# Performance work log

Measured on AMD Instinct MI355X. Metric: run time of the kernel, lower is better.

The kernel has to match this reference:

```python
import jax, jax.numpy as jnp
import numpy as np

B, NS, D, H = 1024, 32, 1024, 4096
LN_EPS = 1e-5


def _layer_norm(x, g, b):
    mu = jnp.mean(x, axis=-1, keepdims=True)
    var = jnp.mean(jnp.square(x - mu), axis=-1, keepdims=True)
    return (x - mu) * jax.lax.rsqrt(var + LN_EPS) * g + b


def setup_inputs() -> dict:
    key = jax.random.key(0)
    ks = jax.random.split(key, 12)
    sc = 0.02
    inp = {
        "x": jax.random.normal(ks[0], (B, D), jnp.float32),
        "S": jax.random.normal(ks[1], (B, NS, D), jnp.float32),
        # route_mlp: Linear(2D, D) -> GELU -> Linear(D, NS)
        "w_r1": jax.random.normal(ks[2], (2 * D, D), jnp.float32) * sc,
        "b_r1": jnp.zeros((D,), jnp.float32),
        "w_r2": jax.random.normal(ks[3], (D, NS), jnp.float32) * sc,
        "b_r2": jnp.zeros((NS,), jnp.float32),
        # GRUCell(D, D): gates ordered [r, z, n] as in torch
        "w_ih": jax.random.normal(ks[4], (D, 3 * D), jnp.float32) * sc,
        "w_hh": jax.random.normal(ks[5], (D, 3 * D), jnp.float32) * sc,
        "b_ih": jnp.zeros((3 * D,), jnp.float32),
        "b_hh": jnp.zeros((3 * D,), jnp.float32),
        # slot_proj: Linear(D, D)
        "w_proj": jax.random.normal(ks[6], (D, D), jnp.float32) * sc,
        "b_proj": jnp.zeros((D,), jnp.float32),
        # ln1 / ffn / ln2
        "ln1_g": jnp.ones((D,), jnp.float32),
        "ln1_b": jnp.zeros((D,), jnp.float32),
        "w_f1": jax.random.normal(ks[7], (D, H), jnp.float32) * sc,
        "b_f1": jnp.zeros((H,), jnp.float32),
        "w_f2": jax.random.normal(ks[8], (H, D), jnp.float32) * sc,
        "b_f2": jnp.zeros((D,), jnp.float32),
        "ln2_g": jnp.ones((D,), jnp.float32),
        "ln2_b": jnp.zeros((D,), jnp.float32),
    }
    return inp


def reference(x, S, w_r1, b_r1, w_r2, b_r2, w_ih, w_hh, b_ih, b_hh,
              w_proj, b_proj, ln1_g, ln1_b, w_f1, b_f1, w_f2, b_f2,
              ln2_g, ln2_b):
    tau = 1.0
    # --- context-aware routing ---
    slot_mean = jnp.mean(S, axis=1)                     # [B, D]
    ctx = jnp.concatenate([x, slot_mean], axis=-1)      # [B, 2D]
    h_r = jax.nn.gelu(ctx @ w_r1 + b_r1, approximate=False)
    r_logits = h_r @ w_r2 + b_r2                        # [B, NS]
    alpha = jax.nn.softmax(r_logits / tau, axis=-1)     # [B, NS]

    # --- GRU slot update: input U = alpha * x broadcast over slots ---
    U = alpha[:, :, None] * x[:, None, :]               # [B, NS, D]
    gi = U @ w_ih + b_ih                                # [B, NS, 3D]
    gh = S @ w_hh + b_hh                                # [B, NS, 3D]
    gi_r, gi_z, gi_n = jnp.split(gi, 3, axis=-1)
    gh_r, gh_z, gh_n = jnp.split(gh, 3, axis=-1)
    r = jax.nn.sigmoid(gi_r + gh_r)
    z = jax.nn.sigmoid(gi_z + gh_z)
    n = jnp.tanh(gi_n + r * gh_n)
    S_new = (1.0 - z) * n + z * S                       # [B, NS, D]

    # --- weighted readout (slot_dropout = 0.0) ---
    slot_context = jnp.sum(alpha[:, :, None] * S_new, axis=1)  # [B, D]
    slot_update = slot_context @ w_proj + b_proj
    x_mid = x + slot_update

    # --- FFN + residual + LayerNorms ---
    h = _layer_norm(x_mid, ln1_g, ln1_b)
    ff = jax.nn.gelu(h @ w_f1 + b_f1, approximate=False) @ w_f2 + b_f2
    x_out = _layer_norm(x_mid + ff, ln2_g, ln2_b)
    return (x_out, S_new, alpha)
```

## Files before the change

kernel.cpp:

```cpp
#include <hip/hip_runtime.h>
#include <hip/hip_bf16.h>

#define BB 1024
#define NSLOT 32
#define DD 1024
#define HH 4096

typedef __bf16 bfx8 __attribute__((ext_vector_type(8)));
typedef float f32x4 __attribute__((ext_vector_type(4)));

__device__ __forceinline__ unsigned short f2bfu(float f) {
  union { float f; unsigned u; } v; v.f = f;
  unsigned r = v.u + 0x7fffu + ((v.u >> 16) & 1u);
  return (unsigned short)(r >> 16);
}
__device__ __forceinline__ float bfu2f(unsigned short u) {
  union { unsigned u; float f; } v; v.u = ((unsigned)u) << 16; return v.f;
}
__device__ __forceinline__ float gelu_f(float x) {
  return 0.5f * x * (1.0f + erff(x * 0.70710678118654752f));
}
__device__ __forceinline__ float sigm(float x) { return 1.0f / (1.0f + expf(-x)); }

__device__ __forceinline__ void async16(const unsigned short* g, unsigned short* l) {
  __builtin_amdgcn_global_load_lds(
      (const __attribute__((address_space(1))) unsigned int*)g,
      (__attribute__((address_space(3))) unsigned int*)l, 16, 0, 0);
}


__global__ __launch_bounds__(256) void cvt_x_ctx(const float* __restrict__ x,
                                                 unsigned short* __restrict__ ctx) {
  int i = blockIdx.x * 256 + threadIdx.x;
  int b = i >> 8;
  int c4 = (i & 255) * 4;
  float4 v = ((const float4*)(x + (size_t)b * DD))[i & 255];
  ushort4 o; o.x = f2bfu(v.x); o.y = f2bfu(v.y); o.z = f2bfu(v.z); o.w = f2bfu(v.w);
  *(ushort4*)&ctx[(size_t)b * (2 * DD) + c4] = o;
}

__global__ __launch_bounds__(256) void cvt4(const float* __restrict__ in,
                                            unsigned short* __restrict__ out, int n4) {
  int i = blockIdx.x * 256 + threadIdx.x;
  if (i >= n4) return;
  float4 v = ((const float4*)in)[i];
  ushort4 o; o.x = f2bfu(v.x); o.y = f2bfu(v.y); o.z = f2bfu(v.z); o.w = f2bfu(v.w);
  ((ushort4*)out)[i] = o;
}

__global__ __launch_bounds__(256) void slot_mean_k(const unsigned short* __restrict__ Sb,
                                                   unsigned short* __restrict__ ctx) {
  int i = blockIdx.x * 256 + threadIdx.x;
  int b = i >> 10, d = i & 1023;
  const unsigned short* p = Sb + (size_t)b * NSLOT * DD + d;
  float s = 0.f;
  #pragma unroll
  for (int sl = 0; sl < NSLOT; sl++) s += bfu2f(p[sl * DD]);
  ctx[(size_t)b * (2 * DD) + DD + d] = f2bfu(s * (1.0f / NSLOT));
}

__global__ __launch_bounds__(256) void transp(const float* __restrict__ in,
                                              unsigned short* __restrict__ out,
                                              int R, int C) {
  __shared__ float t[32][33];
  int tx = threadIdx.x & 31, ty = threadIdx.x >> 5;
  int c0 = blockIdx.x * 32, r0 = blockIdx.y * 32;
  #pragma unroll
  for (int i = 0; i < 4; i++) {
    int r = r0 + ty * 4 + i;
    t[ty * 4 + i][tx] = in[(size_t)r * C + c0 + tx];
  }
  __syncthreads();
  #pragma unroll
  for (int i = 0; i < 4; i++) {
    int c = c0 + ty * 4 + i;
    out[(size_t)c * R + r0 + tx] = f2bfu(t[tx][ty * 4 + i]);
  }
}

template <int EPI>
__global__ __launch_bounds__(256) void gemm_nt(
    const unsigned short* __restrict__ A, int lda,
    const unsigned short* __restrict__ Bt, int ldb, int K,
    const float* __restrict__ bias,
    const float* __restrict__ add, int ldadd,
    float* __restrict__ outF, unsigned short* __restrict__ outB, int ldout) {
  __shared__ __align__(16) unsigned short lA[128 * 40];
  __shared__ __align__(16) unsigned short lB[64 * 40];
  const int tid = threadIdx.x;
  const int wave = tid >> 6, lane = tid & 63;
  const int q = lane >> 4, l15 = lane & 15;
  const int row0 = blockIdx.y * 128;
  const int col0 = blockIdx.x * 64;
  const int ar = tid >> 2;
  const int ac = (tid & 3) * 8;

  f32x4 acc[2][4];
  #pragma unroll
  for (int m = 0; m < 2; m++)
    #pragma unroll
    for (int n = 0; n < 4; n++) acc[m][n] = (f32x4){0.f, 0.f, 0.f, 0.f};

  for (int k0 = 0; k0 < K; k0 += 32) {
    *(uint4*)&lA[ar * 40 + ac] = *(const uint4*)&A[(size_t)(row0 + ar) * lda + k0 + ac];
    *(uint4*)&lA[(ar + 64) * 40 + ac] = *(const uint4*)&A[(size_t)(row0 + ar + 64) * lda + k0 + ac];
    *(uint4*)&lB[ar * 40 + ac] = *(const uint4*)&Bt[(size_t)(col0 + ar) * ldb + k0 + ac];
    __syncthreads();
    bfx8 af[2], bf[4];
    #pragma unroll
    for (int m = 0; m < 2; m++)
      af[m] = *(const bfx8*)&lA[(wave * 32 + m * 16 + l15) * 40 + q * 8];
    #pragma unroll
    for (int n = 0; n < 4; n++)
      bf[n] = *(const bfx8*)&lB[(n * 16 + l15) * 40 + q * 8];
    #pragma unroll
    for (int m = 0; m < 2; m++)
      #pragma unroll
      for (int n = 0; n < 4; n++)
        acc[m][n] = __builtin_amdgcn_mfma_f32_16x16x32_bf16(af[m], bf[n], acc[m][n], 0, 0, 0);
    __syncthreads();
  }

  #pragma unroll
  for (int m = 0; m < 2; m++) {
    #pragma unroll
    for (int n = 0; n < 4; n++) {
      int gr0 = row0 + wave * 32 + m * 16 + q * 4;
      int gc = col0 + n * 16 + l15;
      #pragma unroll
      for (int i = 0; i < 4; i++) {
        int gr = gr0 + i;
        float v = acc[m][n][i];
        if (EPI == 0) {
          outF[(size_t)gr * ldout + gc] = v;
        } else if (EPI == 1) {
          float t = gelu_f(v + bias[gc]);
          outB[(size_t)gr * ldout + gc] = f2bfu(t);
        } else {
          outF[(size_t)gr * ldout + gc] = v + bias[gc] + add[(size_t)gr * ldadd + gc];
        }
      }
    }
  }
}

__global__ __launch_bounds__(256) void gru_gemm(
    const unsigned short* __restrict__ Sb, const unsigned short* __restrict__ Whht,
    const float* __restrict__ alpha, const float* __restrict__ xw,
    const float* __restrict__ b_ih, const float* __restrict__ b_hh,
    const float* __restrict__ Sf, float* __restrict__ Snew,
    unsigned short* __restrict__ sc_b) {
  __shared__ __align__(16) unsigned short lA[2][128 * 32];
  __shared__ __align__(16) unsigned short lB[2][192 * 32];
  const int tid = threadIdx.x;
  const int wave = tid >> 6, lane = tid & 63;
  const int wr = wave >> 1, wc = wave & 1;
  const int q = lane >> 4, l15 = lane & 15;
  const int row0 = blockIdx.y * 128;
  const int col0 = blockIdx.x * 64;
  const int halfA = 128 * 32, halfB = 192 * 32;

  const int lr = lane >> 2, scn = lane & 3;
  const unsigned short* aSrc[2];
  unsigned short* aDst[2];
  #pragma unroll
  for (int j = 0; j < 2; j++) {
    int R0 = (2 * wave + j) * 16;
    int r = R0 + lr;
    int c = scn ^ ((r >> 1) & 3);
    aSrc[j] = Sb + (size_t)(row0 + r) * DD + c * 8;
    aDst[j] = &lA[0][R0 * 32];
  }
  const unsigned short* bSrc[3];
  unsigned short* bDst[3];
  #pragma unroll
  for (int j = 0; j < 3; j++) {
    int R0 = (3 * wave + j) * 16;
    int r = R0 + lr;
    int g = r >> 6, cr = r & 63;
    int c = scn ^ ((r >> 1) & 3);
    bSrc[j] = Whht + ((size_t)g * DD + col0 + cr) * DD + c * 8;
    bDst[j] = &lB[0][R0 * 32];
  }

  int offA[4];
  #pragma unroll
  for (int m = 0; m < 4; m++) {
    int r = wr * 64 + m * 16 + l15;
    offA[m] = r * 32 + (q ^ ((r >> 1) & 3)) * 8;
  }
  int offB[3][2];
  #pragma unroll
  for (int g = 0; g < 3; g++)
    #pragma unroll
    for (int n = 0; n < 2; n++) {
      int r = g * 64 + wc * 32 + n * 16 + l15;
      offB[g][n] = r * 32 + (q ^ ((r >> 1) & 3)) * 8;
    }

  f32x4 acc[3][4][2];
  #pragma unroll
  for (int g = 0; g < 3; g++)
    #pragma unroll
    for (int m = 0; m < 4; m++)
      #pragma unroll
      for (int n = 0; n < 2; n++) acc[g][m][n] = (f32x4){0.f, 0.f, 0.f, 0.f};

  for (int it = 0; it < 16; it++) {
    #pragma unroll
    for (int j = 0; j < 2; j++) {
      async16(aSrc[j], aDst[j]);
      async16(aSrc[j] + 32, aDst[j] + halfA);
      aSrc[j] += 64;
    }
    #pragma unroll
    for (int j = 0; j < 3; j++) {
      async16(bSrc[j], bDst[j]);
      async16(bSrc[j] + 32, bDst[j] + halfB);
      bSrc[j] += 64;
    }
    __syncthreads();
    #pragma unroll
    for (int h = 0; h < 2; h++) {
      bfx8 af[4];
      #pragma unroll
      for (int m = 0; m < 4; m++) af[m] = *(const bfx8*)&lA[h][offA[m]];
      #pragma unroll
      for (int g = 0; g < 3; g++) {
        bfx8 bf0 = *(const bfx8*)&lB[h][offB[g][0]];
        bfx8 bf1 = *(const bfx8*)&lB[h][offB[g][1]];
        #pragma unroll
        for (int m = 0; m < 4; m++) {
          acc[g][m][0] = __builtin_amdgcn_mfma_f32_16x16x32_bf16(af[m], bf0, acc[g][m][0], 0, 0, 0);
          acc[g][m][1] = __builtin_amdgcn_mfma_f32_16x16x32_bf16(af[m], bf1, acc[g][m][1], 0, 0, 0);
        }
      }
    }
    __syncthreads();
  }

  float scp[2][2] = {{0.f, 0.f}, {0.f, 0.f}};
  #pragma unroll
  for (int m = 0; m < 4; m++) {
    #pragma unroll
    for (int i = 0; i < 4; i++) {
      int gr = row0 + wr * 64 + m * 16 + q * 4 + i;
      float a = alpha[gr];
      const float* xwr = xw + (size_t)(gr >> 5) * (3 * DD);
      const float* sfr = Sf + (size_t)gr * DD;
      float* orow = Snew + (size_t)gr * DD;
      #pragma unroll
      for (int n = 0; n < 2; n++) {
        int gc = col0 + wc * 32 + n * 16 + l15;
        float ghr = acc[0][m][n][i] + b_hh[gc];
        float ghz = acc[1][m][n][i] + b_hh[gc + DD];
        float ghn = acc[2][m][n][i] + b_hh[gc + 2 * DD];
        float r = sigm(a * xwr[gc] + b_ih[gc] + ghr);
        float z = sigm(a * xwr[gc + DD] + b_ih[gc + DD] + ghz);
        float nn = tanhf(a * xwr[gc + 2 * DD] + b_ih[gc + 2 * DD] + r * ghn);
        float sv = (1.0f - z) * nn + z * sfr[gc];
        orow[gc] = sv;
        scp[m >> 1][n] += a * sv;
      }
    }
  }
  #pragma unroll
  for (int bh = 0; bh < 2; bh++)
    #pragma unroll
    for (int n = 0; n < 2; n++) {
      float v = scp[bh][n];
      v += __shfl_xor(v, 16);
      v += __shfl_xor(v, 32);
      if (q == 0) {
        int batch = (row0 >> 5) + wr * 2 + bh;
        int gc = col0 + wc * 32 + n * 16 + l15;
        sc_b[(size_t)batch * DD + gc] = f2bfu(v);
      }
    }
}

__global__ __launch_bounds__(256) void route_softmax(
    const unsigned short* __restrict__ h_r, const float* __restrict__ w_r2,
    const float* __restrict__ b_r2, float* __restrict__ alpha_out) {
  int b = blockIdx.x;
  int n = threadIdx.x & 31, c = threadIdx.x >> 5;
  __shared__ float part[8][32];
  __shared__ float logits[32];
  const unsigned short* hr = h_r + (size_t)b * DD;
  float s = 0.f;
  for (int i = 0; i < 128; i++) {
    int k = c * 128 + i;
    s += bfu2f(hr[k]) * w_r2[k * NSLOT + n];
  }
  part[c][n] = s;
  __syncthreads();
  if (threadIdx.x < 32) {
    float t = b_r2[n];
    #pragma unroll
    for (int cc = 0; cc < 8; cc++) t += part[cc][n];
    logits[n] = t;
  }
  __syncthreads();
  if (threadIdx.x < 32) {
    float mx = -1e30f;
    #pragma unroll
    for (int j = 0; j < 32; j++) mx = fmaxf(mx, logits[j]);
    float den = 0.f;
    #pragma unroll
    for (int j = 0; j < 32; j++) den += expf(logits[j] - mx);
    alpha_out[(size_t)b * NSLOT + n] = expf(logits[n] - mx) / den;
  }
}

template <int OUT_BF>
__global__ __launch_bounds__(256) void ln_k(const float* __restrict__ in,
                                            const float* __restrict__ gw,
                                            const float* __restrict__ bw,
                                            float* __restrict__ outF,
                                            unsigned short* __restrict__ outB) {
  int b = blockIdx.x;
  int tid = threadIdx.x;
  float4 v = ((const float4*)(in + (size_t)b * DD))[tid];
  float s = v.x + v.y + v.z + v.w;
  float s2 = v.x * v.x + v.y * v.y + v.z * v.z + v.w * v.w;
  #pragma unroll
  for (int o = 32; o > 0; o >>= 1) { s += __shfl_down(s, o); s2 += __shfl_down(s2, o); }
  __shared__ float as1[4], as2[4];
  int wave = tid >> 6, lane = tid & 63;
  if (lane == 0) { as1[wave] = s; as2[wave] = s2; }
  __syncthreads();
  float t1 = as1[0] + as1[1] + as1[2] + as1[3];
  float t2 = as2[0] + as2[1] + as2[2] + as2[3];
  float mu = t1 * (1.0f / DD);
  float var = t2 * (1.0f / DD) - mu * mu;
  float rstd = rsqrtf(var + 1e-5f);
  int d = tid * 4;
  float o0 = (v.x - mu) * rstd * gw[d] + bw[d];
  float o1 = (v.y - mu) * rstd * gw[d + 1] + bw[d + 1];
  float o2 = (v.z - mu) * rstd * gw[d + 2] + bw[d + 2];
  float o3 = (v.w - mu) * rstd * gw[d + 3] + bw[d + 3];
  if (OUT_BF) {
    ushort4 o; o.x = f2bfu(o0); o.y = f2bfu(o1); o.z = f2bfu(o2); o.w = f2bfu(o3);
    *(ushort4*)&outB[(size_t)b * DD + d] = o;
  } else {
    float4 o; o.x = o0; o.y = o1; o.z = o2; o.w = o3;
    *(float4*)&outF[(size_t)b * DD + d] = o;
  }
}

extern "C" void kernel_launch(void* const* d_in, const int* in_sizes, int n_in,
                              void* d_out, int out_size, void* d_ws, size_t ws_size,
                              hipStream_t stream) {
  const float* x      = (const float*)d_in[0];
  const float* S      = (const float*)d_in[1];
  const float* w_r1   = (const float*)d_in[2];
  const float* b_r1   = (const float*)d_in[3];
  const float* w_r2   = (const float*)d_in[4];
  const float* b_r2   = (const float*)d_in[5];
  const float* w_ih   = (const float*)d_in[6];
  const float* w_hh   = (const float*)d_in[7];
  const float* b_ih   = (const float*)d_in[8];
  const float* b_hh   = (const float*)d_in[9];
  const float* w_proj = (const float*)d_in[10];
  const float* b_proj = (const float*)d_in[11];
  const float* ln1_g  = (const float*)d_in[12];
  const float* ln1_b  = (const float*)d_in[13];
  const float* w_f1   = (const float*)d_in[14];
  const float* b_f1   = (const float*)d_in[15];
  const float* w_f2   = (const float*)d_in[16];
  const float* b_f2   = (const float*)d_in[17];
  const float* ln2_g  = (const float*)d_in[18];
  const float* ln2_b  = (const float*)d_in[19];

  float* out_x = (float*)d_out;
  float* out_S = out_x + (size_t)BB * DD;
  float* out_a = out_S + (size_t)BB * NSLOT * DD;

  char* ws = (char*)d_ws;
  unsigned short* ctx    = (unsigned short*)(ws + 0);
  unsigned short* w_r1t  = (unsigned short*)(ws + 4194304);
  unsigned short* w_iht  = (unsigned short*)(ws + 8388608);
  unsigned short* w_hht  = (unsigned short*)(ws + 14680064);
  unsigned short* w_projt= (unsigned short*)(ws + 20971520);
  unsigned short* w_f1t  = (unsigned short*)(ws + 23068672);
  unsigned short* w_f2t  = (unsigned short*)(ws + 31457280);
  unsigned short* h_r    = (unsigned short*)(ws + 39845888);
  float*          xw     = (float*)(ws + 41943040);
  unsigned short* Sb     = (unsigned short*)(ws + 54525952);
  unsigned short* sc_b   = (unsigned short*)(ws + 0);
  float*          x_mid  = (float*)(ws + 41943040);
  unsigned short* h_ln   = (unsigned short*)(ws + 46137344);
  float*          pre2   = (float*)(ws + 48234496);
  unsigned short* ff1    = (unsigned short*)(ws + 54525952);

  dim3 blk(256);
  cvt_x_ctx<<<1024, blk, 0, stream>>>(x, ctx);
  cvt4<<<32768, blk, 0, stream>>>(S, Sb, (BB * NSLOT * DD) / 4);
  slot_mean_k<<<4096, blk, 0, stream>>>(Sb, ctx);
  transp<<<dim3(32, 64), blk, 0, stream>>>(w_r1, w_r1t, 2 * DD, DD);
  transp<<<dim3(96, 32), blk, 0, stream>>>(w_ih, w_iht, DD, 3 * DD);
  transp<<<dim3(96, 32), blk, 0, stream>>>(w_hh, w_hht, DD, 3 * DD);
  transp<<<dim3(32, 32), blk, 0, stream>>>(w_proj, w_projt, DD, DD);
  transp<<<dim3(128, 32), blk, 0, stream>>>(w_f1, w_f1t, DD, HH);
  transp<<<dim3(32, 128), blk, 0, stream>>>(w_f2, w_f2t, HH, DD);

  gemm_nt<1><<<dim3(16, 8), blk, 0, stream>>>(ctx, 2 * DD, w_r1t, 2 * DD, 2 * DD,
                                              b_r1, nullptr, 0, nullptr, h_r, DD);
  route_softmax<<<1024, blk, 0, stream>>>(h_r, w_r2, b_r2, out_a);

  gemm_nt<0><<<dim3(48, 8), blk, 0, stream>>>(ctx, 2 * DD, w_iht, DD, DD,
                                              nullptr, nullptr, 0, xw, nullptr, 3 * DD);

  gru_gemm<<<dim3(16, 256), blk, 0, stream>>>(Sb, w_hht, out_a, xw, b_ih, b_hh, S,
                                              out_S, sc_b);

  gemm_nt<2><<<dim3(16, 8), blk, 0, stream>>>(sc_b, DD, w_projt, DD, DD,
                                              b_proj, x, DD, x_mid, nullptr, DD);

  ln_k<1><<<1024, blk, 0, stream>>>(x_mid, ln1_g, ln1_b, nullptr, h_ln);
  gemm_nt<1><<<dim3(64, 8), blk, 0, stream>>>(h_ln, DD, w_f1t, DD, DD,
                                              b_f1, nullptr, 0, nullptr, ff1, HH);
  gemm_nt<2><<<dim3(16, 8), blk, 0, stream>>>(ff1, HH, w_f2t, HH, HH,
                                              b_f2, x_mid, DD, pre2, nullptr, DD);
  ln_k<0><<<1024, blk, 0, stream>>>(pre2, ln2_g, ln2_b, out_x, nullptr);
}
```

Measured before the change: 906.6 us.

## Stage GRU epilogue through LDS for coalesced stores, reuse bf16 S, fast math

The GRU epilogue now writes S_new tiles into shared memory and stores them with coalesced float4 writes, replacing the scattered per-element stores. It reads the previous S from the bf16 copy instead of the fp32 input, which removes one fp32 read pass but lowers the precision of the z*S term. Sigmoid and tanh switch to __expf-based versions. The grid is swapped so that blocks covering the same weight columns are adjacent in launch order, which changes L2 reuse.

```diff
diff --git a/kernel.cpp b/kernel.cpp
--- a/kernel.cpp
+++ b/kernel.cpp
@@ -20,7 +20,12 @@
 __device__ __forceinline__ float gelu_f(float x) {
   return 0.5f * x * (1.0f + erff(x * 0.70710678118654752f));
 }
-__device__ __forceinline__ float sigm(float x) { return 1.0f / (1.0f + expf(-x)); }
+__device__ __forceinline__ float sigm_f(float x) { return 1.0f / (1.0f + __expf(-x)); }
+__device__ __forceinline__ float tanh_f(float x) {
+  float e = __expf(-2.0f * fabsf(x));
+  float t = (1.0f - e) / (1.0f + e);
+  return x >= 0.f ? t : -t;
+}
 
 __device__ __forceinline__ void async16(const unsigned short* g, unsigned short* l) {
   __builtin_amdgcn_global_load_lds(
@@ -148,16 +153,16 @@
     const unsigned short* __restrict__ Sb, const unsigned short* __restrict__ Whht,
     const float* __restrict__ alpha, const float* __restrict__ xw,
     const float* __restrict__ b_ih, const float* __restrict__ b_hh,
-    const float* __restrict__ Sf, float* __restrict__ Snew,
-    unsigned short* __restrict__ sc_b) {
-  __shared__ __align__(16) unsigned short lA[2][128 * 32];
-  __shared__ __align__(16) unsigned short lB[2][192 * 32];
+    float* __restrict__ Snew, unsigned short* __restrict__ sc_b) {
+  __shared__ __align__(16) unsigned short smem_us[2 * 128 * 32 + 2 * 192 * 32];
+  unsigned short* lA = smem_us;
+  unsigned short* lB = smem_us + 2 * 128 * 32;
   const int tid = threadIdx.x;
   const int wave = tid >> 6, lane = tid & 63;
   const int wr = wave >> 1, wc = wave & 1;
   const int q = lane >> 4, l15 = lane & 15;
-  const int row0 = blockIdx.y * 128;
-  const int col0 = blockIdx.x * 64;
+  const int row0 = blockIdx.x * 128;
+  const int col0 = blockIdx.y * 64;
   const int halfA = 128 * 32, halfB = 192 * 32;
 
   const int lr = lane >> 2, scn = lane & 3;
@@ -169,7 +174,7 @@
     int r = R0 + lr;
     int c = scn ^ ((r >> 1) & 3);
     aSrc[j] = Sb + (size_t)(row0 + r) * DD + c * 8;
-    aDst[j] = &lA[0][R0 * 32];
+    aDst[j] = &lA[R0 * 32];
   }
   const unsigned short* bSrc[3];
   unsigned short* bDst[3];
@@ -180,7 +185,7 @@
     int g = r >> 6, cr = r & 63;
     int c = scn ^ ((r >> 1) & 3);
     bSrc[j] = Whht + ((size_t)g * DD + col0 + cr) * DD + c * 8;
-    bDst[j] = &lB[0][R0 * 32];
+    bDst[j] = &lB[R0 * 32];
   }
 
   int offA[4];
@@ -224,11 +229,11 @@
     for (int h = 0; h < 2; h++) {
       bfx8 af[4];
       #pragma unroll
-      for (int m = 0; m < 4; m++) af[m] = *(const bfx8*)&lA[h][offA[m]];
+      for (int m = 0; m < 4; m++) af[m] = *(const bfx8*)&lA[h * halfA + offA[m]];
       #pragma unroll
       for (int g = 0; g < 3; g++) {
-        bfx8 bf0 = *(const bfx8*)&lB[h][offB[g][0]];
-        bfx8 bf1 = *(const bfx8*)&lB[h][offB[g][1]];
+        bfx8 bf0 = *(const bfx8*)&lB[h * halfB + offB[g][0]];
+        bfx8 bf1 = *(const bfx8*)&lB[h * halfB + offB[g][1]];
         #pragma unroll
         for (int m = 0; m < 4; m++) {
           acc[g][m][0] = __builtin_amdgcn_mfma_f32_16x16x32_bf16(af[m], bf0, acc[g][m][0], 0, 0, 0);
@@ -239,27 +244,29 @@
     __syncthreads();
   }
 
+  float* fbuf = (float*)smem_us;
   float scp[2][2] = {{0.f, 0.f}, {0.f, 0.f}};
   #pragma unroll
   for (int m = 0; m < 4; m++) {
     #pragma unroll
     for (int i = 0; i < 4; i++) {
-      int gr = row0 + wr * 64 + m * 16 + q * 4 + i;
+      int rl = wr * 64 + m * 16 + q * 4 + i;
+      int gr = row0 + rl;
       float a = alpha[gr];
       const float* xwr = xw + (size_t)(gr >> 5) * (3 * DD);
-      const float* sfr = Sf + (size_t)gr * DD;
-      float* orow = Snew + (size_t)gr * DD;
+      const unsigned short* sbr = Sb + (size_t)gr * DD;
       #pragma unroll
       for (int n = 0; n < 2; n++) {
-        int gc = col0 + wc * 32 + n * 16 + l15;
+        int cl = wc * 32 + n * 16 + l15;
+        int gc = col0 + cl;
         float ghr = acc[0][m][n][i] + b_hh[gc];
         float ghz = acc[1][m][n][i] + b_hh[gc + DD];
         float ghn = acc[2][m][n][i] + b_hh[gc + 2 * DD];
-        float r = sigm(a * xwr[gc] + b_ih[gc] + ghr);
-        float z = sigm(a * xwr[gc + DD] + b_ih[gc + DD] + ghz);
-        float nn = tanhf(a * xwr[gc + 2 * DD] + b_ih[gc + 2 * DD] + r * ghn);
-        float sv = (1.0f - z) * nn + z * sfr[gc];
-        orow[gc] = sv;
+        float r = sigm_f(a * xwr[gc] + b_ih[gc] + ghr);
+        float z = sigm_f(a * xwr[gc + DD] + b_ih[gc + DD] + ghz);
+        float nn = tanh_f(a * xwr[gc + 2 * DD] + b_ih[gc + 2 * DD] + r * ghn);
+        float sv = (1.0f - z) * nn + z * bfu2f(sbr[gc]);
+        fbuf[rl * 68 + cl] = sv;
         scp[m >> 1][n] += a * sv;
       }
     }
@@ -277,6 +284,14 @@
         sc_b[(size_t)batch * DD + gc] = f2bfu(v);
       }
     }
+  __syncthreads();
+  #pragma unroll
+  for (int t8 = 0; t8 < 8; t8++) {
+    int rl = wave * 32 + t8 * 4 + (lane >> 4);
+    int cl = (lane & 15) * 4;
+    float4 v = *(const float4*)&fbuf[rl * 68 + cl];
+    *(float4*)&Snew[(size_t)(row0 + rl) * DD + col0 + cl] = v;
+  }
 }
 
 __global__ __launch_bounds__(256) void route_softmax(
@@ -411,7 +426,7 @@
   gemm_nt<0><<<dim3(48, 8), blk, 0, stream>>>(ctx, 2 * DD, w_iht, DD, DD,
                                               nullptr, nullptr, 0, xw, nullptr, 3 * DD);
 
-  gru_gemm<<<dim3(16, 256), blk, 0, stream>>>(Sb, w_hht, out_a, xw, b_ih, b_hh, S,
+  gru_gemm<<<dim3(256, 16), blk, 0, stream>>>(Sb, w_hht, out_a, xw, b_ih, b_hh,
                                               out_S, sc_b);
 
   gemm_nt<2><<<dim3(16, 8), blk, 0, stream>>>(sc_b, DD, w_projt, DD, DD,
```

Result: slower. 1.058 ms (+16.7%).
